# Performance work log

Hardware: AMD Instinct MI355X
Metric: run time of the kernel (lower is better)

## Reference

```python
import jax, jax.numpy as jnp
import numpy as np

B, T = 128, 50
VOCAB, EMB_D, GRU_H = 10000, 200, 100
HEADS, AHID, THID = 8, 96, 96

def _conv(x, w, b, pad):
    y = jax.lax.conv_general_dilated(x, w, (1, 1), pad,
        dimension_numbers=('NCHW', 'OIHW', 'NCHW'))
    return y + b[None, :, None, None]

def _bn(x, g, b, m, v):
    s = jax.lax.rsqrt(v + 1e-5)
    return (x - m[None, :, None, None]) * (g * s)[None, :, None, None] + b[None, :, None, None]

def _maxpool(x):
    return jax.lax.reduce_window(x, -jnp.inf, jax.lax.max, (1, 1, 2, 2), (1, 1, 2, 2), 'VALID')

def _resize(x):
    # F.interpolate(mode='bilinear', align_corners=False) == half-pixel bilinear, no antialias
    return jax.image.resize(x, (x.shape[0], x.shape[1], 25, 156), 'bilinear', antialias=False)

def _audio_attn(x, wq, bq, wk, bk, wv, bv):
    # x: [B,96,H,W]; wq: [heads,96,96] == stacked per-head 1x1 convs
    Q = jnp.einsum('bchw,noc->bnohw', x, wq) + bq[None, :, :, None, None]
    K = jnp.einsum('bchw,noc->bnohw', x, wk) + bk[None, :, :, None, None]
    V = jnp.einsum('bchw,noc->bnohw', x, wv) + bv[None, :, :, None, None]
    # torch F.softmax with no dim on a 4D tensor defaults to dim=1 (channels) -> axis=2 here
    return jax.nn.softmax(Q * K, axis=2) * V  # [B,heads,96,H,W]

def _text_attn(o, wq, bq, wk, bk, wv, bv):
    # o: [N,100]; wq: [heads,96,100] == stacked per-head Linear layers
    Q = jnp.einsum('nd,hod->nho', o, wq) + bq[None]
    K = jnp.einsum('nd,hod->nho', o, wk) + bk[None]
    V = jnp.einsum('nd,hod->nho', o, wv) + bv[None]
    a = jax.nn.softmax(Q * K, axis=2) * V  # 2D softmax default dim=1 -> over feature axis
    return a.reshape(o.shape[0], -1)  # head-concat order == torch cat along dim=1

def _gru(xs, w_ih, w_hh, b_ih, b_hh):
    # xs: [T,B,200]; torch gate order r, z, n; b_hn applied inside r-gating
    def step(h, x):
        gi = x @ w_ih.T + b_ih
        gh = h @ w_hh.T + b_hh
        ir, iz, inew = jnp.split(gi, 3, axis=1)
        hr, hz, hnew = jnp.split(gh, 3, axis=1)
        r = jax.nn.sigmoid(ir + hr)
        z = jax.nn.sigmoid(iz + hz)
        n = jnp.tanh(inew + r * hnew)
        h2 = (1.0 - z) * n + z * h
        return h2, h2
    h0 = jnp.zeros((xs.shape[1], GRU_H), xs.dtype)
    hT, outs = jax.lax.scan(step, h0, xs)
    return outs, hT

def _forward(tokens, lengths, mfcc_t, mfcc_f, mfcc_c, w1a, b1a, g1a, be1a, m1a, v1a, w1b, b1b, g1b, be1b, m1b, v1b, w2, b2, g2, be2, m2, v2, w3, b3, g3, be3, m3, v3, w4, b4, g4, be4, m4, v4, wq_a1, bq_a1, wk_a1, bk_a1, wv_a1, bv_a1, wq_a2, bq_a2, wk_a2, bk_a2, wv_a2, bv_a2, emb, w_ih, w_hh, b_ih, b_hh, wq_t1, bq_t1, wk_t1, bk_t1, wv_t1, bv_t1, wq_t2, bq_t2, wk_t2, bk_t2, wv_t2, bv_t2, w_fa, b_fa, w_ft, b_ft, w_e, b_e):
    # --- audio CNN stem (eval-mode batchnorm; dropout off) ---
    xa = jax.nn.relu(_bn(_conv(mfcc_t, w1a, b1a, 'VALID'), g1a, be1a, m1a, v1a))
    xb = jax.nn.relu(_bn(_conv(mfcc_f, w1b, b1b, 'VALID'), g1b, be1b, m1b, v1b))
    # NOTE: original source reuses conv1b/bn1b for the third input (faithful to that)
    xc = jax.nn.relu(_bn(_conv(mfcc_c, w1b, b1b, 'VALID'), g1b, be1b, m1b, v1b))
    x = jnp.concatenate([_resize(xa), _resize(xb), _resize(xc)], axis=1)  # [B,24,25,156]
    x = _maxpool(jax.nn.relu(_bn(_conv(x, w2, b2, [(1, 1), (1, 1)]), g2, be2, m2, v2)))  # [B,32,12,78]
    x = _maxpool(jax.nn.relu(_bn(_conv(x, w3, b3, [(1, 1), (1, 1)]), g3, be3, m3, v3)))  # [B,64,6,39]
    x = jax.nn.relu(_bn(_conv(x, w4, b4, [(1, 1), (1, 1)]), g4, be4, m4, v4))            # [B,96,6,39]
    # --- two stacked per-head audio attentions, then per-head spatial GAP ---
    a1 = _audio_attn(x, wq_a1, bq_a1, wk_a1, bk_a1, wv_a1, bv_a1).mean(axis=(-2, -1))  # [B,8,96]
    a2 = _audio_attn(x, wq_a2, bq_a2, wk_a2, bk_a2, wv_a2, bv_a2).mean(axis=(-2, -1))
    # forward() slices heads along the height concat and GAPs -> per head [stage1 96, stage2 96]
    self_attn_audio = jnp.concatenate([a1, a2], axis=2).reshape(x.shape[0], -1)  # [B,1536]
    # --- text branch: embedding + GRU (all lengths == T -> pack/pad is identity) ---
    ex = jnp.swapaxes(emb[tokens], 0, 1)  # [T,B,200]
    outs, h = _gru(ex, w_ih, w_hh, b_ih, b_hh)  # h: [B,100]
    output = jnp.swapaxes(outs, 0, 1).reshape(-1, GRU_H)  # [B*T,100]
    t1 = _text_attn(output, wq_t1, bq_t1, wk_t1, bk_t1, wv_t1, bv_t1)
    t2 = _text_attn(output, wq_t2, bq_t2, wk_t2, bk_t2, wv_t2, bv_t2)
    self_attn_text = jnp.concatenate([t1, t2], axis=1).reshape(x.shape[0], T, -1).sum(axis=1)  # [B,1536]
    # --- cross-modal gated fusion ---
    x_gap = x.mean(axis=(-2, -1))  # [B,96]
    a_text = jax.nn.softmax(x_gap @ w_fa.T + b_fa, axis=1)   # [B,100]
    attn_text_based_audio = a_text * h                        # [B,100]
    a_audio = jax.nn.softmax(h @ w_ft.T + b_ft, axis=1)      # [B,96]
    attn_audio_based_text = a_audio * x_gap                   # [B,96]
    feat = jnp.concatenate([self_attn_audio, self_attn_text,
                            attn_audio_based_text, attn_text_based_audio], axis=1)  # [B,3268]
    return feat @ w_e.T + b_e  # [B,4] emotion logits

def setup_inputs() -> dict:
    key = jax.random.key(0)
    ks = iter(jax.random.split(key, 100))
    nrm = lambda s, sc=0.05: jax.random.normal(next(ks), s, jnp.float32) * sc
    uni = lambda s: jax.random.uniform(next(ks), s, jnp.float32) * 0.5 + 0.5
    d = {}
    d['mfcc_t'] = jax.random.normal(next(ks), (B, 1, 200, 40), jnp.float32)
    d['mfcc_f'] = jax.random.normal(next(ks), (B, 1, 200, 40), jnp.float32)
    d['mfcc_c'] = jax.random.normal(next(ks), (B, 1, 200, 40), jnp.float32)
    d['tokens'] = jax.random.randint(next(ks), (B, T), 0, VOCAB)
    d['lengths'] = jnp.full((B,), T, jnp.int32)
    def bnp(pre, c):
        d['g' + pre] = 1.0 + nrm((c,)); d['be' + pre] = nrm((c,))
        d['m' + pre] = nrm((c,)); d['v' + pre] = uni((c,))
    d['w1a'] = nrm((8, 1, 5, 2), 0.2); d['b1a'] = nrm((8,)); bnp('1a', 8)
    d['w1b'] = nrm((8, 1, 2, 6), 0.2); d['b1b'] = nrm((8,)); bnp('1b', 8)
    d['w2'] = nrm((32, 24, 3, 3), 0.1); d['b2'] = nrm((32,)); bnp('2', 32)
    d['w3'] = nrm((64, 32, 3, 3), 0.1); d['b3'] = nrm((64,)); bnp('3', 64)
    d['w4'] = nrm((96, 64, 3, 3), 0.08); d['b4'] = nrm((96,)); bnp('4', 96)
    for s in ('1', '2'):
        for p in ('q', 'k', 'v'):
            d['w%s_a%s' % (p, s)] = nrm((HEADS, 96, 96), 0.1)
            d['b%s_a%s' % (p, s)] = nrm((HEADS, 96))
    d['emb'] = nrm((VOCAB, EMB_D), 0.1)
    d['w_ih'] = nrm((3 * GRU_H, EMB_D), 0.1); d['w_hh'] = nrm((3 * GRU_H, GRU_H), 0.1)
    d['b_ih'] = nrm((3 * GRU_H,)); d['b_hh'] = nrm((3 * GRU_H,))
    for s in ('1', '2'):
        for p in ('q', 'k', 'v'):
            d['w%s_t%s' % (p, s)] = nrm((HEADS, THID, GRU_H), 0.1)
            d['b%s_t%s' % (p, s)] = nrm((HEADS, THID))
    d['w_fa'] = nrm((100, 96), 0.1); d['b_fa'] = nrm((100,))
    d['w_ft'] = nrm((96, 100), 0.1); d['b_ft'] = nrm((96,))
    d['w_e'] = nrm((4, 2 * HEADS * AHID + 2 * HEADS * THID + 96 + 100), 0.05); d['b_e'] = nrm((4,))
    return d

def reference(mfcc_t, mfcc_f, mfcc_c, tokens, lengths, w1a, b1a, g1a, be1a, m1a, v1a, w1b, b1b, g1b, be1b, m1b, v1b, w2, b2, g2, be2, m2, v2, w3, b3, g3, be3, m3, v3, w4, b4, g4, be4, m4, v4, wq_a1, bq_a1, wk_a1, bk_a1, wv_a1, bv_a1, wq_a2, bq_a2, wk_a2, bk_a2, wv_a2, bv_a2, emb, w_ih, w_hh, b_ih, b_hh, wq_t1, bq_t1, wk_t1, bk_t1, wv_t1, bv_t1, wq_t2, bq_t2, wk_t2, bk_t2, wv_t2, bv_t2, w_fa, b_fa, w_ft, b_ft, w_e, b_e):
    return _forward(tokens, lengths, mfcc_t, mfcc_f, mfcc_c, w1a, b1a, g1a, be1a, m1a, v1a, w1b, b1b, g1b, be1b, m1b, v1b, w2, b2, g2, be2, m2, v2, w3, b3, g3, be3, m3, v3, w4, b4, g4, be4, m4, v4, wq_a1, bq_a1, wk_a1, bk_a1, wv_a1, bv_a1, wq_a2, bq_a2, wk_a2, bk_a2, wv_a2, bv_a2, emb, w_ih, w_hh, b_ih, b_hh, wq_t1, bq_t1, wk_t1, bk_t1, wv_t1, bv_t1, wq_t2, bq_t2, wk_t2, bk_t2, wv_t2, bv_t2, w_fa, b_fa, w_ft, b_ft, w_e, b_e)
```

## Files before the change

### kernel.cpp

```cpp
#include <hip/hip_runtime.h>
#include <math.h>

static constexpr int kB = 128;
static constexpr int kT = 50;

struct TDesc { const float* src; float* dst; int O; int C; int total; };
struct TPack { TDesc d[15]; };
__global__ void k_transpose_pack(TPack p) {
    TDesc t = p.d[blockIdx.y];
    int idx = blockIdx.x * 256 + threadIdx.x;
    if (idx >= t.total) return;
    int o = idx % t.O; int r = idx / t.O; int c = r % t.C; int n = r / t.C;
    t.dst[idx] = t.src[((size_t)n * t.O + o) * t.C + c];
}

__global__ void k_zero(float* __restrict__ a, int n) {
    int i = blockIdx.x * 256 + threadIdx.x;
    if (i < n) a[i] = 0.f;
}

__global__ void k_stem(const float* __restrict__ mt, const float* __restrict__ mf,
                       const float* __restrict__ mc,
                       const float* __restrict__ w1a, const float* __restrict__ b1a,
                       const float* __restrict__ g1a, const float* __restrict__ be1a,
                       const float* __restrict__ m1a, const float* __restrict__ v1a,
                       const float* __restrict__ w1b, const float* __restrict__ b1b,
                       const float* __restrict__ g1b, const float* __restrict__ be1b,
                       const float* __restrict__ m1b, const float* __restrict__ v1b,
                       float* __restrict__ out, int total) {
    int idx = blockIdx.x * blockDim.x + threadIdx.x;
    if (idx >= total) return;
    int ox = idx % 156; int t = idx / 156;
    int oy = t % 25; t /= 25;
    int ch = t % 24; int b = t / 24;
    int grp = ch >> 3, c = ch & 7;
    const float* src; int Hc, Wc;
    const float *wb, *cb, *g, *be, *m, *v;
    if (grp == 0) { src = mt; Hc = 196; Wc = 39; wb = w1a + c * 10;
                    cb = b1a; g = g1a; be = be1a; m = m1a; v = v1a; }
    else          { src = (grp == 1 ? mf : mc); Hc = 199; Wc = 35; wb = w1b + c * 12;
                    cb = b1b; g = g1b; be = be1b; m = m1b; v = v1b; }
    float s = g[c] * rsqrtf(v[c] + 1e-5f);
    float bias = (cb[c] - m[c]) * s + be[c];
    float sy = (oy + 0.5f) * ((float)Hc / 25.f) - 0.5f;
    float sx = (ox + 0.5f) * ((float)Wc / 156.f) - 0.5f;
    float fy0 = floorf(sy), fx0 = floorf(sx);
    float fy = sy - fy0, fx = sx - fx0;
    int y0 = (int)fy0, x0 = (int)fx0;
    int y0c = min(max(y0, 0), Hc - 1), y1c = min(max(y0 + 1, 0), Hc - 1);
    int x0c = min(max(x0, 0), Wc - 1), x1c = min(max(x0 + 1, 0), Wc - 1);
    bool xs = (x1c == x0c), ys = (y1c == y0c);
    const float* p = src + (size_t)b * 8000;
    float t00, t01, t10, t11;
    if (grp == 0) {
        float W[6][3];
        #pragma unroll
        for (int r = 0; r < 6; ++r) {
            int rr = min(y0c + r, 199);
            #pragma unroll
            for (int cc = 0; cc < 3; ++cc)
                W[r][cc] = p[rr * 40 + min(x0c + cc, 39)];
        }
        float a00 = 0.f, a01 = 0.f, a10 = 0.f, a11 = 0.f;
        #pragma unroll
        for (int ky = 0; ky < 5; ++ky)
            #pragma unroll
            for (int kx = 0; kx < 2; ++kx) {
                float wv = wb[ky * 2 + kx];
                a00 += W[ky][kx] * wv;     a01 += W[ky][kx + 1] * wv;
                a10 += W[ky + 1][kx] * wv; a11 += W[ky + 1][kx + 1] * wv;
            }
        t00 = a00;
        t01 = xs ? a00 : a01;
        t10 = ys ? a00 : a10;
        t11 = xs ? (ys ? a00 : a10) : (ys ? a01 : a11);
    } else {
        float W[3][7];
        #pragma unroll
        for (int r = 0; r < 3; ++r) {
            int rr = min(y0c + r, 199);
            #pragma unroll
            for (int cc = 0; cc < 7; ++cc)
                W[r][cc] = p[rr * 40 + min(x0c + cc, 39)];
        }
        float a00 = 0.f, a01 = 0.f, a10 = 0.f, a11 = 0.f;
        #pragma unroll
        for (int ky = 0; ky < 2; ++ky)
            #pragma unroll
            for (int kx = 0; kx < 6; ++kx) {
                float wv = wb[ky * 6 + kx];
                a00 += W[ky][kx] * wv;     a01 += W[ky][kx + 1] * wv;
                a10 += W[ky + 1][kx] * wv; a11 += W[ky + 1][kx + 1] * wv;
            }
        t00 = a00;
        t01 = xs ? a00 : a01;
        t10 = ys ? a00 : a10;
        t11 = xs ? (ys ? a00 : a10) : (ys ? a01 : a11);
    }
    float r00 = fmaxf(t00 * s + bias, 0.f), r01 = fmaxf(t01 * s + bias, 0.f);
    float r10 = fmaxf(t10 * s + bias, 0.f), r11 = fmaxf(t11 * s + bias, 0.f);
    out[idx] = r00 * (1.f - fy) * (1.f - fx) + r01 * (1.f - fy) * fx
             + r10 * fy * (1.f - fx) + r11 * fy * fx;
}

template<int CIN, int CI_T, int H, int W, int ROWS, int NPX>
__global__ void __launch_bounds__(256) k_conv3x3_tiled(
    const float* __restrict__ in, const float* __restrict__ wT,
    const float* __restrict__ cb, const float* __restrict__ g,
    const float* __restrict__ be, const float* __restrict__ m,
    const float* __restrict__ v, float* __restrict__ out, int COUT) {
    constexpr int WP = W + 2;
    constexpr int RP = ROWS + 2;
    constexpr int STAGE = CI_T * RP * WP;
    __shared__ float sx[STAGE];
    __shared__ float sw[CI_T * 9 * 8];
    const int b = blockIdx.x, rt = blockIdx.y, oc0 = blockIdx.z * 8;
    const int row0 = rt * ROWS;
    const int tid = threadIdx.x;

    int off[NPX]; bool val[NPX];
    #pragma unroll
    for (int j = 0; j < NPX; ++j) {
        int px = tid + j * 256;
        int oy = px / W, ox = px - oy * W;
        bool ok = (px < ROWS * W) && (row0 + oy < H);
        val[j] = ok;
        off[j] = ok ? (oy * WP + ox) : 0;
    }

    float acc[NPX][8];
    #pragma unroll
    for (int j = 0; j < NPX; ++j)
        #pragma unroll
        for (int o = 0; o < 8; ++o) acc[j][o] = 0.f;

    for (int c0 = 0; c0 < CIN; c0 += CI_T) {
        __syncthreads();
        for (int e = tid; e < STAGE; e += 256) {
            int ci = e / (RP * WP);
            int rem = e - ci * RP * WP;
            int r = rem / WP;
            int xx = rem - r * WP;
            int iy = row0 - 1 + r;
            int ix = xx - 1;
            float vv = 0.f;
            if (iy >= 0 && iy < H && ix >= 0 && ix < W)
                vv = in[((size_t)(b * CIN + c0 + ci) * H + iy) * W + ix];
            sx[e] = vv;
        }
        for (int e = tid; e < CI_T * 9 * 8; e += 256) {
            int rk = e >> 3;
            int o = e & 7;
            sw[e] = wT[((size_t)c0 * 9 + rk) * COUT + oc0 + o];
        }
        __syncthreads();
        #pragma unroll 1
        for (int cl = 0; cl < CI_T; ++cl) {
            const float* sxc = sx + cl * RP * WP;
            #pragma unroll
            for (int k = 0; k < 9; ++k) {
                const int ky = k / 3, kx = k % 3;
                const float4 wa = *(const float4*)(sw + (cl * 9 + k) * 8);
                const float4 wb = *(const float4*)(sw + (cl * 9 + k) * 8 + 4);
                #pragma unroll
                for (int j = 0; j < NPX; ++j) {
                    float xv = sxc[off[j] + ky * WP + kx];
                    acc[j][0] += xv * wa.x; acc[j][1] += xv * wa.y;
                    acc[j][2] += xv * wa.z; acc[j][3] += xv * wa.w;
                    acc[j][4] += xv * wb.x; acc[j][5] += xv * wb.y;
                    acc[j][6] += xv * wb.z; acc[j][7] += xv * wb.w;
                }
            }
        }
    }
    float sc[8], bi[8];
    #pragma unroll
    for (int o = 0; o < 8; ++o) {
        float s = g[oc0 + o] * rsqrtf(v[oc0 + o] + 1e-5f);
        sc[o] = s; bi[o] = (cb[oc0 + o] - m[oc0 + o]) * s + be[oc0 + o];
    }
    #pragma unroll
    for (int j = 0; j < NPX; ++j) if (val[j]) {
        int px = tid + j * 256;
        int oy = row0 + px / W, ox = px % W;
        #pragma unroll
        for (int o = 0; o < 8; ++o)
            out[((size_t)(b * COUT + oc0 + o) * H + oy) * W + ox] =
                fmaxf(acc[j][o] * sc[o] + bi[o], 0.f);
    }
}

__global__ void k_maxpool(const float* __restrict__ in, float* __restrict__ out,
                          int C, int Hin, int Win, int Hout, int Wout, int total) {
    int idx = blockIdx.x * blockDim.x + threadIdx.x;
    if (idx >= total) return;
    int ox = idx % Wout; int t = idx / Wout;
    int oy = t % Hout; t /= Hout;
    int c = t % C; int b = t / C;
    const float* p = in + ((size_t)(b * C + c) * Hin + 2 * oy) * Win + 2 * ox;
    float m0 = fmaxf(p[0], p[1]);
    float m1 = fmaxf(p[Win], p[Win + 1]);
    out[idx] = fmaxf(m0, m1);
}

__global__ void __launch_bounds__(256) k_xgap(const float* __restrict__ x,
                                              float* __restrict__ xgap) {
    int b = blockIdx.x, tid = threadIdx.x;
    int wave = tid >> 6, lane = tid & 63;
    for (int c = wave; c < 96; c += 4) {
        const float* row = x + ((size_t)b * 96 + c) * 234;
        float s = 0.f;
        for (int p = lane; p < 234; p += 64) s += row[p];
        #pragma unroll
        for (int off = 1; off < 64; off <<= 1) s += __shfl_xor(s, off);
        if (lane == 0) xgap[b * 96 + c] = s * (1.f / 234.f);
    }
}

__global__ void __launch_bounds__(256, 4) k_audio_attn(
    const float* __restrict__ x,
    const float* __restrict__ wq1, const float* __restrict__ bq1,
    const float* __restrict__ wk1, const float* __restrict__ bk1,
    const float* __restrict__ wv1, const float* __restrict__ bv1,
    const float* __restrict__ wq2, const float* __restrict__ bq2,
    const float* __restrict__ wk2, const float* __restrict__ bk2,
    const float* __restrict__ wv2, const float* __restrict__ bv2,
    float* __restrict__ afeat) {
    const int b = blockIdx.x >> 2, pt = blockIdx.x & 3;
    const int n = blockIdx.y, stage = blockIdx.z;
    const float* wq = (stage ? wq2 : wq1) + n * 9216;
    const float* wk = (stage ? wk2 : wk1) + n * 9216;
    const float* wv = (stage ? wv2 : wv1) + n * 9216;
    const float* bqn = (stage ? bq2 : bq1) + n * 96;
    const float* bkn = (stage ? bk2 : bk1) + n * 96;
    const float* bvn = (stage ? bv2 : bv1) + n * 96;
    const int tid = threadIdx.x;
    const int to = tid >> 4, tp = tid & 15;
    const int ob = to * 6;
    const int p0 = pt * 64;

    __shared__ float sx[96 * 64];
    __shared__ float sw[1536];
    __shared__ float sred[1536];

    {
        const float* xb = x + (size_t)b * (96 * 234) + p0;
        for (int e = tid; e < 96 * 64; e += 256) {
            int c = e >> 6, p = e & 63;
            sx[e] = (p0 + p < 234) ? xb[c * 234 + p] : 0.f;
        }
    }

    float qa[6][4], ka[6][4];
    #pragma unroll
    for (int j = 0; j < 6; ++j) {
        float bq_ = bqn[ob + j], bk_ = bkn[ob + j];
        #pragma unroll
        for (int i = 0; i < 4; ++i) { qa[j][i] = bq_; ka[j][i] = bk_; }
    }

    for (int c0 = 0; c0 < 96; c0 += 8) {
        __syncthreads();
        {
            const int base = c0 * 96;
            for (int e4 = tid; e4 < 384; e4 += 256) {
                int mat = (e4 >= 192);
                int r4 = e4 - mat * 192;
                const float* wsrc = mat ? wk : wq;
                *(float4*)(sw + e4 * 4) = *(const float4*)(wsrc + base + r4 * 4);
            }
        }
        __syncthreads();
        #pragma unroll 2
        for (int cc = 0; cc < 8; ++cc) {
            float4 x4 = *(const float4*)(sx + (c0 + cc) * 64 + tp * 4);
            const float* wr = sw + cc * 96 + ob;
            float2 q01 = *(const float2*)(wr);
            float2 q23 = *(const float2*)(wr + 2);
            float2 q45 = *(const float2*)(wr + 4);
            float2 k01 = *(const float2*)(wr + 768);
            float2 k23 = *(const float2*)(wr + 770);
            float2 k45 = *(const float2*)(wr + 772);
            float wqv[6] = {q01.x, q01.y, q23.x, q23.y, q45.x, q45.y};
            float wkv[6] = {k01.x, k01.y, k23.x, k23.y, k45.x, k45.y};
            #pragma unroll
            for (int j = 0; j < 6; ++j) {
                qa[j][0] += wqv[j] * x4.x; qa[j][1] += wqv[j] * x4.y;
                qa[j][2] += wqv[j] * x4.z; qa[j][3] += wqv[j] * x4.w;
                ka[j][0] += wkv[j] * x4.x; ka[j][1] += wkv[j] * x4.y;
                ka[j][2] += wkv[j] * x4.z; ka[j][3] += wkv[j] * x4.w;
            }
        }
    }

    float pmx[4] = {-1e30f, -1e30f, -1e30f, -1e30f};
    #pragma unroll
    for (int j = 0; j < 6; ++j)
        #pragma unroll
        for (int i = 0; i < 4; ++i) {
            float sv = qa[j][i] * ka[j][i];
            qa[j][i] = sv;
            pmx[i] = fmaxf(pmx[i], sv);
        }
    __syncthreads();
    #pragma unroll
    for (int i = 0; i < 4; ++i) sred[to * 64 + tp * 4 + i] = pmx[i];
    __syncthreads();
    float m_[4];
    #pragma unroll
    for (int i = 0; i < 4; ++i) {
        float mm = -1e30f;
        for (int t = 0; t < 16; ++t) mm = fmaxf(mm, sred[t * 64 + tp * 4 + i]);
        m_[i] = mm;
    }
    __syncthreads();
    float z[4] = {0.f, 0.f, 0.f, 0.f};
    #pragma unroll
    for (int j = 0; j < 6; ++j)
        #pragma unroll
        for (int i = 0; i < 4; ++i) {
            float e = __expf(qa[j][i] - m_[i]);
            qa[j][i] = e;
            z[i] += e;
        }
    #pragma unroll
    for (int i = 0; i < 4; ++i) sred[to * 64 + tp * 4 + i] = z[i];
    __syncthreads();
    float rz[4];
    #pragma unroll
    for (int i = 0; i < 4; ++i) {
        float zs = 0.f;
        for (int t = 0; t < 16; ++t) zs += sred[t * 64 + tp * 4 + i];
        rz[i] = (p0 + tp * 4 + i < 234) ? 1.f / zs : 0.f;
    }

    float va[6][4];
    #pragma unroll
    for (int j = 0; j < 6; ++j) {
        float bv_ = bvn[ob + j];
        #pragma unroll
        for (int i = 0; i < 4; ++i) va[j][i] = bv_;
    }
    for (int c0 = 0; c0 < 96; c0 += 16) {
        __syncthreads();
        {
            const float* wsrc = wv + c0 * 96;
            for (int e4 = tid; e4 < 384; e4 += 256)
                *(float4*)(sw + e4 * 4) = *(const float4*)(wsrc + e4 * 4);
        }
        __syncthreads();
        #pragma unroll 2
        for (int cc = 0; cc < 16; ++cc) {
            float4 x4 = *(const float4*)(sx + (c0 + cc) * 64 + tp * 4);
            const float* wr = sw + cc * 96 + ob;
            float2 v01 = *(const float2*)(wr);
            float2 v23 = *(const float2*)(wr + 2);
            float2 v45 = *(const float2*)(wr + 4);
            float wvv[6] = {v01.x, v01.y, v23.x, v23.y, v45.x, v45.y};
            #pragma unroll
            for (int j = 0; j < 6; ++j) {
                va[j][0] += wvv[j] * x4.x; va[j][1] += wvv[j] * x4.y;
                va[j][2] += wvv[j] * x4.z; va[j][3] += wvv[j] * x4.w;
            }
        }
    }

    __syncthreads();
    #pragma unroll
    for (int j = 0; j < 6; ++j) {
        float po = qa[j][0] * rz[0] * va[j][0]
                 + qa[j][1] * rz[1] * va[j][1]
                 + qa[j][2] * rz[2] * va[j][2]
                 + qa[j][3] * rz[3] * va[j][3];
        sred[(ob + j) * 16 + tp] = po;
    }
    __syncthreads();
    if (tid < 96) {
        float ssum = 0.f;
        #pragma unroll
        for (int t = 0; t < 16; ++t) ssum += sred[tid * 16 + t];
        atomicAdd(afeat + b * 1536 + n * 192 + stage * 96 + tid, ssum * (1.f / 234.f));
    }
}

__global__ void __launch_bounds__(320) k_gi(const int* __restrict__ tokens,
        const float* __restrict__ emb, const float* __restrict__ w_ih,
        const float* __restrict__ b_ih, float* __restrict__ GI) {
    int r0 = blockIdx.x * 8;
    int tid = threadIdx.x;
    __shared__ float er[8][200];
    for (int e = tid; e < 1600; e += 320) {
        int r = e / 200, c = e - r * 200;
        er[r][c] = emb[(size_t)tokens[r0 + r] * 200 + c];
    }
    __syncthreads();
    if (tid < 300) {
        float acc[8];
        float bv = b_ih[tid];
        #pragma unroll
        for (int r = 0; r < 8; ++r) acc[r] = bv;
        for (int k4 = 0; k4 < 50; ++k4) {
            float4 w4 = *(const float4*)(w_ih + (size_t)tid * 200 + k4 * 4);
            #pragma unroll
            for (int r = 0; r < 8; ++r) {
                float4 x4 = *(const float4*)&er[r][k4 * 4];
                acc[r] += w4.x * x4.x + w4.y * x4.y + w4.z * x4.z + w4.w * x4.w;
            }
        }
        #pragma unroll
        for (int r = 0; r < 8; ++r)
            GI[(size_t)(r0 + r) * 300 + tid] = acc[r];
    }
}

__global__ void __launch_bounds__(320) k_gru_all(const float* __restrict__ GI,
        const float* __restrict__ w_hh, const float* __restrict__ b_hh,
        float* __restrict__ outs) {
    int b = blockIdx.x, tid = threadIdx.x;
    __shared__ float hs[100];
    __shared__ float gH[300];
    float4 wreg[25];
    float bias = 0.f;
    if (tid < 300) {
        bias = b_hh[tid];
        #pragma unroll
        for (int k4 = 0; k4 < 25; ++k4)
            wreg[k4] = *(const float4*)(w_hh + (size_t)tid * 100 + k4 * 4);
    }
    if (tid < 100) hs[tid] = 0.f;
    __syncthreads();
    for (int t = 0; t < kT; ++t) {
        if (tid < 300) {
            float gh = bias;
            #pragma unroll
            for (int k4 = 0; k4 < 25; ++k4) {
                float4 h4 = *(const float4*)&hs[k4 * 4];
                gh += wreg[k4].x * h4.x + wreg[k4].y * h4.y
                    + wreg[k4].z * h4.z + wreg[k4].w * h4.w;
            }
            gH[tid] = gh;
        }
        __syncthreads();
        if (tid < 100) {
            const float* gi = GI + ((size_t)b * kT + t) * 300;
            float r = 1.f / (1.f + expf(-(gi[tid] + gH[tid])));
            float z = 1.f / (1.f + expf(-(gi[100 + tid] + gH[100 + tid])));
            float nn = tanhf(gi[200 + tid] + r * gH[200 + tid]);
            float h2 = (1.f - z) * nn + z * hs[tid];
            hs[tid] = h2;
            outs[((size_t)b * kT + t) * 100 + tid] = h2;
        }
        __syncthreads();
    }
}

__global__ void __launch_bounds__(128) k_text_attn(const float* __restrict__ outs,
    const float* __restrict__ wq1, const float* __restrict__ bq1,
    const float* __restrict__ wk1, const float* __restrict__ bk1,
    const float* __restrict__ wv1, const float* __restrict__ bv1,
    const float* __restrict__ wq2, const float* __restrict__ bq2,
    const float* __restrict__ wk2, const float* __restrict__ bk2,
    const float* __restrict__ wv2, const float* __restrict__ bv2,
    float* __restrict__ tfeat) {
    int b = blockIdx.x, stage = blockIdx.y, n = blockIdx.z;
    const float* wq = stage ? wq2 : wq1; const float* bq = stage ? bq2 : bq1;
    const float* wk = stage ? wk2 : wk1; const float* bk = stage ? bk2 : bk1;
    const float* wv = stage ? wv2 : wv1; const float* bv = stage ? bv2 : bv1;
    int tid = threadIdx.x;
    bool act = tid < 96;
    int oo = act ? tid : 0;
    const float* wqc = wq + n * 9600 + oo;
    const float* wkc = wk + n * 9600 + oo;
    const float* wvc = wv + n * 9600 + oo;
    float bqv = act ? bq[n * 96 + tid] : 0.f;
    float bkv = act ? bk[n * 96 + tid] : 0.f;
    float bvv = act ? bv[n * 96 + tid] : 0.f;
    __shared__ float rows[10][100];
    __shared__ float wredM[2][10], wredS[2][10];
    float acc = 0.f;
    int wave = tid >> 6, lane = tid & 63;
    for (int tile = 0; tile < 5; ++tile) {
        int t0 = tile * 10;
        __syncthreads();
        for (int e = tid; e < 1000; e += 128) {
            int tt = e / 100, c = e - tt * 100;
            rows[tt][c] = outs[((size_t)b * kT + t0 + tt) * 100 + c];
        }
        __syncthreads();
        float q[10], k[10], v[10];
        #pragma unroll
        for (int tt = 0; tt < 10; ++tt) { q[tt] = bqv; k[tt] = bkv; v[tt] = bvv; }
        for (int c4 = 0; c4 < 25; ++c4) {
            int cb = c4 * 4 * 96;
            float q0 = wqc[cb], q1 = wqc[cb + 96], q2 = wqc[cb + 192], q3 = wqc[cb + 288];
            float k0 = wkc[cb], k1 = wkc[cb + 96], k2 = wkc[cb + 192], k3 = wkc[cb + 288];
            float v0 = wvc[cb], v1 = wvc[cb + 96], v2 = wvc[cb + 192], v3 = wvc[cb + 288];
            #pragma unroll
            for (int tt = 0; tt < 10; ++tt) {
                float4 x4 = *(const float4*)&rows[tt][c4 * 4];
                q[tt] += q0 * x4.x + q1 * x4.y + q2 * x4.z + q3 * x4.w;
                k[tt] += k0 * x4.x + k1 * x4.y + k2 * x4.z + k3 * x4.w;
                v[tt] += v0 * x4.x + v1 * x4.y + v2 * x4.z + v3 * x4.w;
            }
        }
        float s[10], e_[10];
        #pragma unroll
        for (int tt = 0; tt < 10; ++tt) s[tt] = act ? q[tt] * k[tt] : -1e30f;
        #pragma unroll
        for (int tt = 0; tt < 10; ++tt) {
            float m = s[tt];
            #pragma unroll
            for (int off = 1; off < 64; off <<= 1) m = fmaxf(m, __shfl_xor(m, off));
            if (lane == 0) wredM[wave][tt] = m;
        }
        __syncthreads();
        #pragma unroll
        for (int tt = 0; tt < 10; ++tt) {
            float mx = fmaxf(wredM[0][tt], wredM[1][tt]);
            e_[tt] = expf(s[tt] - mx);
        }
        #pragma unroll
        for (int tt = 0; tt < 10; ++tt) {
            float sm = e_[tt];
            #pragma unroll
            for (int off = 1; off < 64; off <<= 1) sm += __shfl_xor(sm, off);
            if (lane == 0) wredS[wave][tt] = sm;
        }
        __syncthreads();
        #pragma unroll
        for (int tt = 0; tt < 10; ++tt) {
            float sm = wredS[0][tt] + wredS[1][tt];
            acc += e_[tt] / sm * v[tt];
        }
    }
    if (act) tfeat[b * 1536 + stage * 768 + n * 96 + tid] = acc;
}

__global__ void __launch_bounds__(128) k_final(const float* __restrict__ xgap,
    const float* __restrict__ outs, const float* __restrict__ afeat,
    const float* __restrict__ tfeat,
    const float* __restrict__ w_fa, const float* __restrict__ b_fa,
    const float* __restrict__ w_ft, const float* __restrict__ b_ft,
    const float* __restrict__ w_e, const float* __restrict__ b_e,
    float* __restrict__ out) {
    int b = blockIdx.x; int tid = threadIdx.x;
    __shared__ float xg[96], hv[100], st[100], sa[96], aat[96], atba[100];
    __shared__ float redm[2], reds[2];
    if (tid < 96) xg[tid] = xgap[b * 96 + tid];
    if (tid < 100) hv[tid] = outs[(size_t)(b * kT + kT - 1) * 100 + tid];
    __syncthreads();
    if (tid < 100) {
        float acc = b_fa[tid];
        const float* wr = w_fa + tid * 96;
        for (int c = 0; c < 96; ++c) acc += wr[c] * xg[c];
        st[tid] = acc;
    }
    if (tid < 96) {
        float acc = b_ft[tid];
        const float* wr = w_ft + tid * 100;
        for (int c = 0; c < 100; ++c) acc += wr[c] * hv[c];
        sa[tid] = acc;
    }
    __syncthreads();
    if (tid == 0) {
        float mxv = -1e30f; for (int i = 0; i < 100; ++i) mxv = fmaxf(mxv, st[i]);
        float s = 0.f; for (int i = 0; i < 100; ++i) s += expf(st[i] - mxv);
        redm[0] = mxv; reds[0] = s;
    }
    if (tid == 1) {
        float mxv = -1e30f; for (int i = 0; i < 96; ++i) mxv = fmaxf(mxv, sa[i]);
        float s = 0.f; for (int i = 0; i < 96; ++i) s += expf(sa[i] - mxv);
        redm[1] = mxv; reds[1] = s;
    }
    __syncthreads();
    if (tid < 100) atba[tid] = expf(st[tid] - redm[0]) / reds[0] * hv[tid];
    if (tid < 96)  aat[tid]  = expf(sa[tid] - redm[1]) / reds[1] * xg[tid];
    __syncthreads();
    float a0 = 0.f, a1 = 0.f, a2 = 0.f, a3 = 0.f;
    for (int col = tid; col < 3268; col += 128) {
        float f;
        if (col < 1536)      f = afeat[b * 1536 + col];
        else if (col < 3072) f = tfeat[b * 1536 + col - 1536];
        else if (col < 3168) f = aat[col - 3072];
        else                 f = atba[col - 3168];
        a0 += w_e[col] * f;            a1 += w_e[3268 + col] * f;
        a2 += w_e[2 * 3268 + col] * f; a3 += w_e[3 * 3268 + col] * f;
    }
    __shared__ float r4[4][128];
    r4[0][tid] = a0; r4[1][tid] = a1; r4[2][tid] = a2; r4[3][tid] = a3;
    __syncthreads();
    if (tid < 4) {
        float s = 0.f;
        for (int i = 0; i < 128; ++i) s += r4[tid][i];
        out[b * 4 + tid] = s + b_e[tid];
    }
}

extern "C" void kernel_launch(void* const* d_in, const int* in_sizes, int n_in,
                              void* d_out, int out_size, void* d_ws, size_t ws_size,
                              hipStream_t stream) {
    (void)in_sizes; (void)n_in; (void)out_size; (void)ws_size;
    const float* mfcc_t = (const float*)d_in[0];
    const float* mfcc_f = (const float*)d_in[1];
    const float* mfcc_c = (const float*)d_in[2];
    const int*   tokens = (const int*)d_in[3];
    const float *w1a = (const float*)d_in[5],  *b1a = (const float*)d_in[6],
                *g1a = (const float*)d_in[7],  *be1a = (const float*)d_in[8],
                *m1a = (const float*)d_in[9],  *v1a = (const float*)d_in[10];
    const float *w1b = (const float*)d_in[11], *b1b = (const float*)d_in[12],
                *g1b = (const float*)d_in[13], *be1b = (const float*)d_in[14],
                *m1b = (const float*)d_in[15], *v1b = (const float*)d_in[16];
    const float *w2 = (const float*)d_in[17], *b2 = (const float*)d_in[18],
                *g2 = (const float*)d_in[19], *be2 = (const float*)d_in[20],
                *m2 = (const float*)d_in[21], *v2 = (const float*)d_in[22];
    const float *w3 = (const float*)d_in[23], *b3 = (const float*)d_in[24],
                *g3 = (const float*)d_in[25], *be3 = (const float*)d_in[26],
                *m3 = (const float*)d_in[27], *v3 = (const float*)d_in[28];
    const float *w4 = (const float*)d_in[29], *b4 = (const float*)d_in[30],
                *g4 = (const float*)d_in[31], *be4 = (const float*)d_in[32],
                *m4 = (const float*)d_in[33], *v4 = (const float*)d_in[34];
    const float *wq_a1 = (const float*)d_in[35], *bq_a1 = (const float*)d_in[36],
                *wk_a1 = (const float*)d_in[37], *bk_a1 = (const float*)d_in[38],
                *wv_a1 = (const float*)d_in[39], *bv_a1 = (const float*)d_in[40];
    const float *wq_a2 = (const float*)d_in[41], *bq_a2 = (const float*)d_in[42],
                *wk_a2 = (const float*)d_in[43], *bk_a2 = (const float*)d_in[44],
                *wv_a2 = (const float*)d_in[45], *bv_a2 = (const float*)d_in[46];
    const float *emb  = (const float*)d_in[47];
    const float *w_ih = (const float*)d_in[48], *w_hh = (const float*)d_in[49],
                *b_ih = (const float*)d_in[50], *b_hh = (const float*)d_in[51];
    const float *wq_t1 = (const float*)d_in[52], *bq_t1 = (const float*)d_in[53],
                *wk_t1 = (const float*)d_in[54], *bk_t1 = (const float*)d_in[55],
                *wv_t1 = (const float*)d_in[56], *bv_t1 = (const float*)d_in[57];
    const float *wq_t2 = (const float*)d_in[58], *bq_t2 = (const float*)d_in[59],
                *wk_t2 = (const float*)d_in[60], *bk_t2 = (const float*)d_in[61],
                *wv_t2 = (const float*)d_in[62], *bv_t2 = (const float*)d_in[63];
    const float *w_fa = (const float*)d_in[64], *b_fa = (const float*)d_in[65],
                *w_ft = (const float*)d_in[66], *b_ft = (const float*)d_in[67],
                *w_e  = (const float*)d_in[68], *b_e  = (const float*)d_in[69];

    float* ws = (float*)d_ws;
    const size_t Z0 = 0;
    const size_t Z1 = 22091776ull;
    const size_t OUTS  = 34072576ull;
    const size_t AFEAT = 34712576ull;
    const size_t TFEAT = 34909184ull;
    const size_t XGAP  = 35105792ull;
    const size_t WT    = 35118080ull;
    float* X1 = ws + Z1;
    float* C2 = ws + Z0;  float* P2 = ws + Z1;
    float* C3 = ws + Z0;  float* P3 = ws + Z1;
    float* X4 = ws + Z0;  float* GI = ws + Z1;
    float* outs  = ws + OUTS;
    float* afeat = ws + AFEAT;
    float* tfeat = ws + TFEAT;
    float* xgap  = ws + XGAP;
    float* wqa1t = ws + WT;
    float* wka1t = wqa1t + 73728; float* wva1t = wka1t + 73728;
    float* wqa2t = wva1t + 73728; float* wka2t = wqa2t + 73728; float* wva2t = wka2t + 73728;
    float* wqt1t = wva2t + 73728;
    float* wkt1t = wqt1t + 76800; float* wvt1t = wkt1t + 76800;
    float* wqt2t = wvt1t + 76800; float* wkt2t = wqt2t + 76800; float* wvt2t = wkt2t + 76800;
    float* wT2 = outs;
    float* wT3 = outs + 6912;
    float* wT4 = outs + 25344;

    TPack tp;
    tp.d[0]  = {wq_a1, wqa1t, 96, 96, 73728};
    tp.d[1]  = {wk_a1, wka1t, 96, 96, 73728};
    tp.d[2]  = {wv_a1, wva1t, 96, 96, 73728};
    tp.d[3]  = {wq_a2, wqa2t, 96, 96, 73728};
    tp.d[4]  = {wk_a2, wka2t, 96, 96, 73728};
    tp.d[5]  = {wv_a2, wva2t, 96, 96, 73728};
    tp.d[6]  = {w2, wT2, 32, 216, 6912};
    tp.d[7]  = {w3, wT3, 64, 288, 18432};
    tp.d[8]  = {w4, wT4, 96, 576, 55296};
    tp.d[9]  = {wq_t1, wqt1t, 96, 100, 76800};
    tp.d[10] = {wk_t1, wkt1t, 96, 100, 76800};
    tp.d[11] = {wv_t1, wvt1t, 96, 100, 76800};
    tp.d[12] = {wq_t2, wqt2t, 96, 100, 76800};
    tp.d[13] = {wk_t2, wkt2t, 96, 100, 76800};
    tp.d[14] = {wv_t2, wvt2t, 96, 100, 76800};
    k_transpose_pack<<<dim3(300, 15), 256, 0, stream>>>(tp);

    k_zero<<<768, 256, 0, stream>>>(afeat, 196608);

    k_stem<<<46800, 256, 0, stream>>>(mfcc_t, mfcc_f, mfcc_c,
        w1a, b1a, g1a, be1a, m1a, v1a,
        w1b, b1b, g1b, be1b, m1b, v1b, X1, 11980800);
    k_conv3x3_tiled<24, 8, 25, 156, 9, 6><<<dim3(128, 3, 4), 256, 0, stream>>>(
        X1, wT2, b2, g2, be2, m2, v2, C2, 32);
    k_maxpool<<<14976, 256, 0, stream>>>(C2, P2, 32, 25, 156, 12, 78, 3833856);
    k_conv3x3_tiled<32, 8, 12, 78, 12, 4><<<dim3(128, 1, 8), 256, 0, stream>>>(
        P2, wT3, b3, g3, be3, m3, v3, C3, 64);
    k_maxpool<<<7488, 256, 0, stream>>>(C3, P3, 64, 12, 78, 6, 39, 1916928);
    k_conv3x3_tiled<64, 16, 6, 39, 6, 1><<<dim3(128, 1, 12), 256, 0, stream>>>(
        P3, wT4, b4, g4, be4, m4, v4, X4, 96);

    k_xgap<<<kB, 256, 0, stream>>>(X4, xgap);

    k_audio_attn<<<dim3(kB * 4, 8, 2), 256, 0, stream>>>(X4,
        wqa1t, bq_a1, wka1t, bk_a1, wva1t, bv_a1,
        wqa2t, bq_a2, wka2t, bk_a2, wva2t, bv_a2, afeat);

    k_gi<<<kB * kT / 8, 320, 0, stream>>>(tokens, emb, w_ih, b_ih, GI);
    k_gru_all<<<kB, 320, 0, stream>>>(GI, w_hh, b_hh, outs);
    k_text_attn<<<dim3(kB, 2, 8), 128, 0, stream>>>(outs,
        wqt1t, bq_t1, wkt1t, bk_t1, wvt1t, bv_t1,
        wqt2t, bq_t2, wkt2t, bk_t2, wvt2t, bv_t2, tfeat);

    k_final<<<kB, 128, 0, stream>>>(xgap, outs, afeat, tfeat,
                                    w_fa, b_fa, w_ft, b_ft, w_e, b_e, (float*)d_out);
}
```

Measured before the change: 1.480 ms.

## Stream x tiles in audio attention, fuse GAP and zero-init into existing kernels

The audio attention kernel no longer stages the whole 96x64 input tile in shared memory. It streams 16-channel slices alongside the Q/K and V weight chunks, and keeps the normalized softmax probabilities in shared memory instead of registers. The global average pool is folded into the first audio-attention block via atomics, and the afeat/xgap zeroing is folded into the transpose-pack launch, which removes two kernel launches. In exchange, x is re-read from global memory for both the QK and V passes, and extra atomics are added for xgap.

```diff
diff --git a/kernel.cpp b/kernel.cpp
--- a/kernel.cpp
+++ b/kernel.cpp
@@ -6,17 +6,18 @@
 
 struct TDesc { const float* src; float* dst; int O; int C; int total; };
 struct TPack { TDesc d[15]; };
-__global__ void k_transpose_pack(TPack p) {
+__global__ void k_transpose_pack(TPack p, float* __restrict__ za, float* __restrict__ zx) {
+    if (blockIdx.y == 15) {
+        for (int i = blockIdx.x * 256 + threadIdx.x; i < 208896; i += 76800) {
+            if (i < 196608) za[i] = 0.f; else zx[i - 196608] = 0.f;
+        }
+        return;
+    }
     TDesc t = p.d[blockIdx.y];
     int idx = blockIdx.x * 256 + threadIdx.x;
     if (idx >= t.total) return;
     int o = idx % t.O; int r = idx / t.O; int c = r % t.C; int n = r / t.C;
     t.dst[idx] = t.src[((size_t)n * t.O + o) * t.C + c];
-}
-
-__global__ void k_zero(float* __restrict__ a, int n) {
-    int i = blockIdx.x * 256 + threadIdx.x;
-    if (i < n) a[i] = 0.f;
 }
 
 __global__ void k_stem(const float* __restrict__ mt, const float* __restrict__ mf,
@@ -203,20 +204,6 @@
     out[idx] = fmaxf(m0, m1);
 }
 
-__global__ void __launch_bounds__(256) k_xgap(const float* __restrict__ x,
-                                              float* __restrict__ xgap) {
-    int b = blockIdx.x, tid = threadIdx.x;
-    int wave = tid >> 6, lane = tid & 63;
-    for (int c = wave; c < 96; c += 4) {
-        const float* row = x + ((size_t)b * 96 + c) * 234;
-        float s = 0.f;
-        for (int p = lane; p < 234; p += 64) s += row[p];
-        #pragma unroll
-        for (int off = 1; off < 64; off <<= 1) s += __shfl_xor(s, off);
-        if (lane == 0) xgap[b * 96 + c] = s * (1.f / 234.f);
-    }
-}
-
 __global__ void __launch_bounds__(256, 4) k_audio_attn(
     const float* __restrict__ x,
     const float* __restrict__ wq1, const float* __restrict__ bq1,
@@ -225,7 +212,7 @@
     const float* __restrict__ wq2, const float* __restrict__ bq2,
     const float* __restrict__ wk2, const float* __restrict__ bk2,
     const float* __restrict__ wv2, const float* __restrict__ bv2,
-    float* __restrict__ afeat) {
+    float* __restrict__ afeat, float* __restrict__ xgap) {
     const int b = blockIdx.x >> 2, pt = blockIdx.x & 3;
     const int n = blockIdx.y, stage = blockIdx.z;
     const float* wq = (stage ? wq2 : wq1) + n * 9216;
@@ -239,17 +226,14 @@
     const int ob = to * 6;
     const int p0 = pt * 64;
 
-    __shared__ float sx[96 * 64];
-    __shared__ float sw[1536];
-    __shared__ float sred[1536];
-
-    {
-        const float* xb = x + (size_t)b * (96 * 234) + p0;
-        for (int e = tid; e < 96 * 64; e += 256) {
-            int c = e >> 6, p = e & 63;
-            sx[e] = (p0 + p < 234) ? xb[c * 234 + p] : 0.f;
-        }
-    }
+    __shared__ float sxc[16 * 64];
+    __shared__ float sw[3072];
+    __shared__ float sP[96 * 64];
+
+    float* sred = sw;
+
+    const float* xb = x + (size_t)b * (96 * 234) + p0;
+    const bool gapblk = (n == 0 && stage == 0);
 
     float qa[6][4], ka[6][4];
     #pragma unroll
@@ -259,28 +243,40 @@
         for (int i = 0; i < 4; ++i) { qa[j][i] = bq_; ka[j][i] = bk_; }
     }
 
-    for (int c0 = 0; c0 < 96; c0 += 8) {
+    for (int c0 = 0; c0 < 96; c0 += 16) {
         __syncthreads();
         {
-            const int base = c0 * 96;
-            for (int e4 = tid; e4 < 384; e4 += 256) {
-                int mat = (e4 >= 192);
-                int r4 = e4 - mat * 192;
-                const float* wsrc = mat ? wk : wq;
-                *(float4*)(sw + e4 * 4) = *(const float4*)(wsrc + base + r4 * 4);
-            }
-        }
-        __syncthreads();
-        #pragma unroll 2
-        for (int cc = 0; cc < 8; ++cc) {
-            float4 x4 = *(const float4*)(sx + (c0 + cc) * 64 + tp * 4);
+            #pragma unroll
+            for (int it = 0; it < 2; ++it) {
+                int e2 = tid + it * 256;
+                int r = e2 >> 5, c2 = (e2 & 31) * 2;
+                float2 v = make_float2(0.f, 0.f);
+                if (p0 + c2 < 234) v = *(const float2*)(xb + (c0 + r) * 234 + c2);
+                *(float2*)(sxc + r * 64 + c2) = v;
+            }
+        }
+        for (int e4 = tid; e4 < 768; e4 += 256) {
+            const float* src = (e4 < 384) ? (wq + c0 * 96 + e4 * 4)
+                                          : (wk + c0 * 96 + (e4 - 384) * 4);
+            *(float4*)(sw + e4 * 4) = *(const float4*)(src);
+        }
+        __syncthreads();
+        if (gapblk) {
+            int r = tid >> 4, q = (tid & 15) * 4;
+            const float* sr = sxc + r * 64 + q;
+            atomicAdd(&xgap[b * 96 + c0 + r],
+                      (sr[0] + sr[1] + sr[2] + sr[3]) * (1.f / 234.f));
+        }
+        #pragma unroll 4
+        for (int cc = 0; cc < 16; ++cc) {
+            float4 x4 = *(const float4*)(sxc + cc * 64 + tp * 4);
             const float* wr = sw + cc * 96 + ob;
             float2 q01 = *(const float2*)(wr);
             float2 q23 = *(const float2*)(wr + 2);
             float2 q45 = *(const float2*)(wr + 4);
-            float2 k01 = *(const float2*)(wr + 768);
-            float2 k23 = *(const float2*)(wr + 770);
-            float2 k45 = *(const float2*)(wr + 772);
+            float2 k01 = *(const float2*)(wr + 1536);
+            float2 k23 = *(const float2*)(wr + 1538);
+            float2 k45 = *(const float2*)(wr + 1540);
             float wqv[6] = {q01.x, q01.y, q23.x, q23.y, q45.x, q45.y};
             float wkv[6] = {k01.x, k01.y, k23.x, k23.y, k45.x, k45.y};
             #pragma unroll
@@ -333,6 +329,12 @@
         for (int t = 0; t < 16; ++t) zs += sred[t * 64 + tp * 4 + i];
         rz[i] = (p0 + tp * 4 + i < 234) ? 1.f / zs : 0.f;
     }
+    #pragma unroll
+    for (int j = 0; j < 6; ++j) {
+        float4 pw = make_float4(qa[j][0] * rz[0], qa[j][1] * rz[1],
+                                qa[j][2] * rz[2], qa[j][3] * rz[3]);
+        *(float4*)(sP + (ob + j) * 64 + tp * 4) = pw;
+    }
 
     float va[6][4];
     #pragma unroll
@@ -344,14 +346,21 @@
     for (int c0 = 0; c0 < 96; c0 += 16) {
         __syncthreads();
         {
-            const float* wsrc = wv + c0 * 96;
-            for (int e4 = tid; e4 < 384; e4 += 256)
-                *(float4*)(sw + e4 * 4) = *(const float4*)(wsrc + e4 * 4);
-        }
-        __syncthreads();
-        #pragma unroll 2
+            #pragma unroll
+            for (int it = 0; it < 2; ++it) {
+                int e2 = tid + it * 256;
+                int r = e2 >> 5, c2 = (e2 & 31) * 2;
+                float2 v = make_float2(0.f, 0.f);
+                if (p0 + c2 < 234) v = *(const float2*)(xb + (c0 + r) * 234 + c2);
+                *(float2*)(sxc + r * 64 + c2) = v;
+            }
+        }
+        for (int e4 = tid; e4 < 384; e4 += 256)
+            *(float4*)(sw + e4 * 4) = *(const float4*)(wv + c0 * 96 + e4 * 4);
+        __syncthreads();
+        #pragma unroll 4
         for (int cc = 0; cc < 16; ++cc) {
-            float4 x4 = *(const float4*)(sx + (c0 + cc) * 64 + tp * 4);
+            float4 x4 = *(const float4*)(sxc + cc * 64 + tp * 4);
             const float* wr = sw + cc * 96 + ob;
             float2 v01 = *(const float2*)(wr);
             float2 v23 = *(const float2*)(wr + 2);
@@ -368,10 +377,9 @@
     __syncthreads();
     #pragma unroll
     for (int j = 0; j < 6; ++j) {
-        float po = qa[j][0] * rz[0] * va[j][0]
-                 + qa[j][1] * rz[1] * va[j][1]
-                 + qa[j][2] * rz[2] * va[j][2]
-                 + qa[j][3] * rz[3] * va[j][3];
+        float4 pj = *(const float4*)(sP + (ob + j) * 64 + tp * 4);
+        float po = pj.x * va[j][0] + pj.y * va[j][1]
+                 + pj.z * va[j][2] + pj.w * va[j][3];
         sred[(ob + j) * 16 + tp] = po;
     }
     __syncthreads();
@@ -680,9 +688,7 @@
     tp.d[12] = {wq_t2, wqt2t, 96, 100, 76800};
     tp.d[13] = {wk_t2, wkt2t, 96, 100, 76800};
     tp.d[14] = {wv_t2, wvt2t, 96, 100, 76800};
-    k_transpose_pack<<<dim3(300, 15), 256, 0, stream>>>(tp);
-
-    k_zero<<<768, 256, 0, stream>>>(afeat, 196608);
+    k_transpose_pack<<<dim3(300, 16), 256, 0, stream>>>(tp, afeat, xgap);
 
     k_stem<<<46800, 256, 0, stream>>>(mfcc_t, mfcc_f, mfcc_c,
         w1a, b1a, g1a, be1a, m1a, v1a,
@@ -696,11 +702,9 @@
     k_conv3x3_tiled<64, 16, 6, 39, 6, 1><<<dim3(128, 1, 12), 256, 0, stream>>>(
         P3, wT4, b4, g4, be4, m4, v4, X4, 96);
 
-    k_xgap<<<kB, 256, 0, stream>>>(X4, xgap);
-
     k_audio_attn<<<dim3(kB * 4, 8, 2), 256, 0, stream>>>(X4,
         wqa1t, bq_a1, wka1t, bk_a1, wva1t, bv_a1,
-        wqa2t, bq_a2, wka2t, bk_a2, wva2t, bv_a2, afeat);
+        wqa2t, bq_a2, wka2t, bk_a2, wva2t, bv_a2, afeat, xgap);
 
     k_gi<<<kB * kT / 8, 320, 0, stream>>>(tokens, emb, w_ih, b_ih, GI);
     k_gru_all<<<kB, 320, 0, stream>>>(GI, w_hh, b_hh, outs);
```

New measurement: 1.465 ms. About the same (-1.0%).
